# Optimization experiments

Measured on AMD Instinct MI355X. Metric: run time of the kernel, lower is better.

The kernel has to match this reference:

```python
import jax, jax.numpy as jnp
import numpy as np


def setup_inputs() -> dict:
    key = jax.random.key(0)
    ks = jax.random.split(key, 5)
    B, S, D, L = 16, 256, 768, 32
    return {
        "head": jax.random.normal(ks[0], (B, S, D), dtype=jnp.float32),
        "dep": jax.random.normal(ks[1], (B, S, D), dtype=jnp.float32),
        "label_U_diag": jax.random.normal(ks[2], (L, D), dtype=jnp.float32) * 0.02,
        "label_W": jax.random.normal(ks[3], (L, 2 * D), dtype=jnp.float32) * 0.02,
        "label_b": jax.random.normal(ks[4], (L,), dtype=jnp.float32) * 0.02,
    }


def reference(head, dep, label_U_diag, label_W, label_b):
    # head, dep: [b, s, d]; label_U_diag: [l, d]; label_W: [l, 2d]; label_b: [l]
    d = head.shape[-1]
    # Bilinear term with diagonal U: t1[b,l,i,o] = sum_d head[b,i,d]*U[l,d]*dep[b,o,d]
    t1 = jnp.einsum('bid,ld,bod->blio', head, label_U_diag, dep)
    # Linear term: W @ concat(head_i, dep_o) = W_h @ head_i + W_d @ dep_o
    W_h, W_d = label_W[:, :d], label_W[:, d:]
    t2_h = jnp.einsum('ld,bid->bli', W_h, head)  # [b, l, s]
    t2_d = jnp.einsum('ld,bod->blo', W_d, dep)   # [b, l, s]
    return t1 + t2_h[:, :, :, None] + t2_d[:, :, None, :] + label_b[None, :, None, None]
```

## Files before the change

kernel.cpp:

```cpp
#include <hip/hip_runtime.h>
#include <hip/hip_bf16.h>
#include <stdint.h>


#define B_ 16
#define S_ 256
#define D_ 768
#define L_ 32

typedef unsigned short ushort_t;
typedef __attribute__((ext_vector_type(4))) float f32x4;
typedef __attribute__((ext_vector_type(8))) short s16x8;

typedef __attribute__((address_space(1))) const unsigned int guint;
typedef __attribute__((address_space(3))) unsigned int luint;

__device__ __forceinline__ void async_load16(const ushort_t* g, ushort_t* l) {
  __builtin_amdgcn_global_load_lds((guint*)g, (luint*)l, 16, 0, 0);
}

__device__ __forceinline__ unsigned int pack_bf16(float f0, float f1) {
  unsigned int u0 = __builtin_bit_cast(unsigned int, f0) + 0x8000u;
  unsigned int u1 = __builtin_bit_cast(unsigned int, f1) + 0x8000u;
  return __builtin_amdgcn_perm(u1, u0, 0x07060302);
}

__global__ __launch_bounds__(256) void prep_kernel(
    const float* __restrict__ head, const float* __restrict__ dep,
    const float* __restrict__ labelW, ushort_t* __restrict__ depb,
    float* __restrict__ t2h, float* __restrict__ t2d) {
  const int wave = threadIdx.x >> 6;
  const int lane = threadIdx.x & 63;
  const int g = blockIdx.x * 4 + wave;
  const int sel = g >> 10;
  const int idx = g & 1023;
  const int b = idx >> 6;
  const int row0 = (idx & 63) * 4;
  const float* src = sel ? dep : head;
  float* t2x = sel ? t2d : t2h;
  const int d0 = lane * 12;

  float h[4][12];
  const float* rp = src + ((size_t)(b * S_ + row0)) * D_ + d0;
#pragma unroll
  for (int r = 0; r < 4; ++r) {
    float4 v0 = *(const float4*)(rp + (size_t)r * D_);
    float4 v1 = *(const float4*)(rp + (size_t)r * D_ + 4);
    float4 v2 = *(const float4*)(rp + (size_t)r * D_ + 8);
    h[r][0] = v0.x; h[r][1] = v0.y; h[r][2] = v0.z; h[r][3] = v0.w;
    h[r][4] = v1.x; h[r][5] = v1.y; h[r][6] = v1.z; h[r][7] = v1.w;
    h[r][8] = v2.x; h[r][9] = v2.y; h[r][10] = v2.z; h[r][11] = v2.w;
  }
  if (sel) {
#pragma unroll
    for (int r = 0; r < 4; ++r) {
      uint2 q0 = {pack_bf16(h[r][0], h[r][1]), pack_bf16(h[r][2], h[r][3])};
      uint2 q1 = {pack_bf16(h[r][4], h[r][5]), pack_bf16(h[r][6], h[r][7])};
      uint2 q2 = {pack_bf16(h[r][8], h[r][9]), pack_bf16(h[r][10], h[r][11])};
      uint2* dp = (uint2*)(depb + ((size_t)(b * S_ + row0 + r)) * D_ + d0);
      dp[0] = q0; dp[1] = q1; dp[2] = q2;
    }
  }
  const float* wbase = labelW + sel * D_ + d0;
  for (int l = 0; l < L_; ++l) {
    const float* wp = wbase + (size_t)l * (2 * D_);
    float4 w0 = *(const float4*)(wp);
    float4 w1 = *(const float4*)(wp + 4);
    float4 w2 = *(const float4*)(wp + 8);
    float w[12] = {w0.x, w0.y, w0.z, w0.w, w1.x, w1.y, w1.z, w1.w,
                   w2.x, w2.y, w2.z, w2.w};
    float p0 = 0.f, p1 = 0.f, p2 = 0.f, p3 = 0.f;
#pragma unroll
    for (int j = 0; j < 12; ++j) {
      p0 += h[0][j] * w[j];
      p1 += h[1][j] * w[j];
      p2 += h[2][j] * w[j];
      p3 += h[3][j] * w[j];
    }
#pragma unroll
    for (int off = 32; off >= 1; off >>= 1) {
      p0 += __shfl_xor(p0, off);
      p1 += __shfl_xor(p1, off);
      p2 += __shfl_xor(p2, off);
      p3 += __shfl_xor(p3, off);
    }
    if (lane < 4) {
      float v = lane == 0 ? p0 : lane == 1 ? p1 : lane == 2 ? p2 : p3;
      t2x[((size_t)(b * L_ + l)) * S_ + row0 + lane] = v;
    }
  }
}

__global__ __launch_bounds__(256, 2) void main_kernel(
    const float* __restrict__ head, const ushort_t* __restrict__ depb,
    const float* __restrict__ U, const float* __restrict__ bias,
    const float* __restrict__ t2h, const float* __restrict__ t2d,
    float* __restrict__ out) {
  __shared__ ushort_t As[128 * 32];
  __shared__ ushort_t Bs[256 * 32];
  __shared__ float T2[384];

  const int bid = blockIdx.x;
  const int ic = bid & 1;
  const int bl = bid >> 1;
  const int l = bl & (L_ - 1);
  const int b = bl >> 5;
  const int ti = ic * 128;
  const int t = threadIdx.x;
  const int lane = t & 63;
  const int wave = t >> 6;
  const int m_base = (wave >> 1) * 64;
  const int n_base = (wave & 1) * 128;

  for (int i = t; i < 384; i += 256)
    T2[i] = (i < 128) ? t2h[((size_t)(b * L_ + l)) * S_ + ti + i]
                      : t2d[((size_t)(b * L_ + l)) * S_ + (i - 128)];
  const float bv = bias[l];

  const int row0 = t >> 2;
  const int kq = (t & 3) * 8;
  const float* hp0 = head + ((size_t)(b * S_ + ti + row0)) * D_ + kq;
  const float* hp1 = hp0 + (size_t)64 * D_;
  const float* Up = U + (size_t)l * D_ + kq;
  const ushort_t* dp = depb + ((size_t)(b * S_ + row0)) * D_ + kq;
  ushort_t* asw0 = As + t * 8;
  ushort_t* asw1 = As + t * 8 + 2048;

  f32x4 acc[4][8];
#pragma unroll
  for (int i = 0; i < 4; ++i)
#pragma unroll
    for (int j = 0; j < 8; ++j) acc[i][j] = {0.f, 0.f, 0.f, 0.f};

  const ushort_t* ar = As + ((m_base + (lane & 15)) * 32 + (lane >> 4) * 8);
  const ushort_t* br = Bs + ((n_base + (lane & 15)) * 32 + (lane >> 4) * 8);

  for (int kk = 0; kk < D_; kk += 32) {
    __syncthreads();
#pragma unroll
    for (int j = 0; j < 4; ++j)
      async_load16(dp + kk + (size_t)j * 64 * D_, Bs + j * 2048 + t * 8);
    float4 h0 = *(const float4*)(hp0 + kk);
    float4 h1 = *(const float4*)(hp0 + kk + 4);
    float4 h2 = *(const float4*)(hp1 + kk);
    float4 h3 = *(const float4*)(hp1 + kk + 4);
    float4 u0 = *(const float4*)(Up + kk);
    float4 u1 = *(const float4*)(Up + kk + 4);
    uint4 w0, w1;
    w0.x = pack_bf16(h0.x * u0.x, h0.y * u0.y);
    w0.y = pack_bf16(h0.z * u0.z, h0.w * u0.w);
    w0.z = pack_bf16(h1.x * u1.x, h1.y * u1.y);
    w0.w = pack_bf16(h1.z * u1.z, h1.w * u1.w);
    w1.x = pack_bf16(h2.x * u0.x, h2.y * u0.y);
    w1.y = pack_bf16(h2.z * u0.z, h2.w * u0.w);
    w1.z = pack_bf16(h3.x * u1.x, h3.y * u1.y);
    w1.w = pack_bf16(h3.z * u1.z, h3.w * u1.w);
    *(uint4*)asw0 = w0;
    *(uint4*)asw1 = w1;
    __syncthreads();

    s16x8 af[4], bf[8];
#pragma unroll
    for (int rt = 0; rt < 4; ++rt) af[rt] = *(const s16x8*)(ar + rt * 512);
#pragma unroll
    for (int ct = 0; ct < 8; ++ct) bf[ct] = *(const s16x8*)(br + ct * 512);
#pragma unroll
    for (int rt = 0; rt < 4; ++rt)
#pragma unroll
      for (int ct = 0; ct < 8; ++ct)
        acc[rt][ct] = __builtin_amdgcn_mfma_f32_16x16x32_bf16(af[rt], bf[ct],
                                                              acc[rt][ct], 0, 0, 0);
  }

  const int colg = lane & 15;
  const int rgrp = lane >> 4;
  float* ob = out + (((size_t)(b * L_ + l)) * S_ + ti) * S_;
#pragma unroll
  for (int rt = 0; rt < 4; ++rt) {
    const int r0 = m_base + rt * 16 + rgrp * 4;
#pragma unroll
    for (int ct = 0; ct < 8; ++ct) {
      const int c = n_base + ct * 16 + colg;
      const float addc = T2[128 + c] + bv;
      float* p = ob + (size_t)r0 * S_ + c;
#pragma unroll
      for (int r = 0; r < 4; ++r)
        p[(size_t)r * S_] = acc[rt][ct][r] + T2[r0 + r] + addc;
    }
  }
}

extern "C" void kernel_launch(void* const* d_in, const int* in_sizes, int n_in,
                              void* d_out, int out_size, void* d_ws, size_t ws_size,
                              hipStream_t stream) {
  const float* head = (const float*)d_in[0];
  const float* dep = (const float*)d_in[1];
  const float* U = (const float*)d_in[2];
  const float* W = (const float*)d_in[3];
  const float* bias = (const float*)d_in[4];
  float* out = (float*)d_out;

  ushort_t* depb = (ushort_t*)d_ws;
  float* t2h = (float*)((char*)d_ws + (size_t)B_ * S_ * D_ * 2);
  float* t2d = t2h + (size_t)B_ * L_ * S_;

  prep_kernel<<<512, 256, 0, stream>>>(head, dep, W, depb, t2h, t2d);
  main_kernel<<<B_ * L_ * 2, 256, 0, stream>>>(head, depb, U, bias, t2h, t2d, out);
}
```

Baseline: 249.4 us.

## Double-buffer LDS tiles to overlap next-tile loads with MFMA compute

The main GEMM loop now uses two LDS buffers for the A and B tiles. It issues the async dep loads and head/U global loads for the next K-slice before running MFMAs on the current slice, then packs and stores the next A tile afterward. This removes one barrier per iteration and hides global-load latency behind matrix math. In exchange, LDS usage doubles and live registers increase, which may affect occupancy.

```diff
diff --git a/kernel.cpp b/kernel.cpp
--- a/kernel.cpp
+++ b/kernel.cpp
@@ -96,8 +96,8 @@
     const float* __restrict__ U, const float* __restrict__ bias,
     const float* __restrict__ t2h, const float* __restrict__ t2d,
     float* __restrict__ out) {
-  __shared__ ushort_t As[128 * 32];
-  __shared__ ushort_t Bs[256 * 32];
+  __shared__ ushort_t As[2 * 128 * 32];
+  __shared__ ushort_t Bs[2 * 256 * 32];
   __shared__ float T2[384];
 
   const int bid = blockIdx.x;
@@ -123,8 +123,6 @@
   const float* hp1 = hp0 + (size_t)64 * D_;
   const float* Up = U + (size_t)l * D_ + kq;
   const ushort_t* dp = depb + ((size_t)(b * S_ + row0)) * D_ + kq;
-  ushort_t* asw0 = As + t * 8;
-  ushort_t* asw1 = As + t * 8 + 2048;
 
   f32x4 acc[4][8];
 #pragma unroll
@@ -135,17 +133,16 @@
   const ushort_t* ar = As + ((m_base + (lane & 15)) * 32 + (lane >> 4) * 8);
   const ushort_t* br = Bs + ((n_base + (lane & 15)) * 32 + (lane >> 4) * 8);
 
-  for (int kk = 0; kk < D_; kk += 32) {
-    __syncthreads();
-#pragma unroll
-    for (int j = 0; j < 4; ++j)
-      async_load16(dp + kk + (size_t)j * 64 * D_, Bs + j * 2048 + t * 8);
-    float4 h0 = *(const float4*)(hp0 + kk);
-    float4 h1 = *(const float4*)(hp0 + kk + 4);
-    float4 h2 = *(const float4*)(hp1 + kk);
-    float4 h3 = *(const float4*)(hp1 + kk + 4);
-    float4 u0 = *(const float4*)(Up + kk);
-    float4 u1 = *(const float4*)(Up + kk + 4);
+#pragma unroll
+  for (int j = 0; j < 4; ++j)
+    async_load16(dp + (size_t)j * 64 * D_, Bs + j * 2048 + t * 8);
+  {
+    float4 h0 = *(const float4*)(hp0);
+    float4 h1 = *(const float4*)(hp0 + 4);
+    float4 h2 = *(const float4*)(hp1);
+    float4 h3 = *(const float4*)(hp1 + 4);
+    float4 u0 = *(const float4*)(Up);
+    float4 u1 = *(const float4*)(Up + 4);
     uint4 w0, w1;
     w0.x = pack_bf16(h0.x * u0.x, h0.y * u0.y);
     w0.y = pack_bf16(h0.z * u0.z, h0.w * u0.w);
@@ -155,21 +152,58 @@
     w1.y = pack_bf16(h2.z * u0.z, h2.w * u0.w);
     w1.z = pack_bf16(h3.x * u1.x, h3.y * u1.y);
     w1.w = pack_bf16(h3.z * u1.z, h3.w * u1.w);
-    *(uint4*)asw0 = w0;
-    *(uint4*)asw1 = w1;
+    *(uint4*)(As + t * 8) = w0;
+    *(uint4*)(As + t * 8 + 2048) = w1;
+  }
+
+  for (int k = 0; k < 24; ++k) {
+    const int kk = k * 32;
+    const int cur = k & 1;
+    const int nxt = cur ^ 1;
     __syncthreads();
 
+    float4 h0, h1, h2, h3, u0, u1;
+    const bool more = (k + 1) < 24;
+    if (more) {
+#pragma unroll
+      for (int j = 0; j < 4; ++j)
+        async_load16(dp + kk + 32 + (size_t)j * 64 * D_,
+                     Bs + nxt * 8192 + j * 2048 + t * 8);
+      h0 = *(const float4*)(hp0 + kk + 32);
+      h1 = *(const float4*)(hp0 + kk + 36);
+      h2 = *(const float4*)(hp1 + kk + 32);
+      h3 = *(const float4*)(hp1 + kk + 36);
+      u0 = *(const float4*)(Up + kk + 32);
+      u1 = *(const float4*)(Up + kk + 36);
+    }
+
     s16x8 af[4], bf[8];
-#pragma unroll
-    for (int rt = 0; rt < 4; ++rt) af[rt] = *(const s16x8*)(ar + rt * 512);
-#pragma unroll
-    for (int ct = 0; ct < 8; ++ct) bf[ct] = *(const s16x8*)(br + ct * 512);
+    const ushort_t* arc = ar + cur * 4096;
+    const ushort_t* brc = br + cur * 8192;
+#pragma unroll
+    for (int rt = 0; rt < 4; ++rt) af[rt] = *(const s16x8*)(arc + rt * 512);
+#pragma unroll
+    for (int ct = 0; ct < 8; ++ct) bf[ct] = *(const s16x8*)(brc + ct * 512);
 #pragma unroll
     for (int rt = 0; rt < 4; ++rt)
 #pragma unroll
       for (int ct = 0; ct < 8; ++ct)
         acc[rt][ct] = __builtin_amdgcn_mfma_f32_16x16x32_bf16(af[rt], bf[ct],
                                                               acc[rt][ct], 0, 0, 0);
+
+    if (more) {
+      uint4 w0, w1;
+      w0.x = pack_bf16(h0.x * u0.x, h0.y * u0.y);
+      w0.y = pack_bf16(h0.z * u0.z, h0.w * u0.w);
+      w0.z = pack_bf16(h1.x * u1.x, h1.y * u1.y);
+      w0.w = pack_bf16(h1.z * u1.z, h1.w * u1.w);
+      w1.x = pack_bf16(h2.x * u0.x, h2.y * u0.y);
+      w1.y = pack_bf16(h2.z * u0.z, h2.w * u0.w);
+      w1.z = pack_bf16(h3.x * u1.x, h3.y * u1.y);
+      w1.w = pack_bf16(h3.z * u1.z, h3.w * u1.w);
+      *(uint4*)(As + nxt * 4096 + t * 8) = w0;
+      *(uint4*)(As + nxt * 4096 + t * 8 + 2048) = w1;
+    }
   }
 
   const int colg = lane & 15;
```

After: 250.8 us. No clear change (+0.6%).
